# Kernel optimization log

Measured on AMD Instinct MI355X. Metric: run time of the kernel, lower is better.

Reference implementation:

```python
import jax, jax.numpy as jnp
import numpy as np

B, S, D, H = 2, 2048, 1024, 16
DK = D // H

def setup_inputs() -> dict:
    key = jax.random.key(0)
    ks = jax.random.split(key, 11)
    s = 1.0 / np.sqrt(D)
    return {
        "q": jax.random.normal(ks[0], (B, S, D), jnp.float32),
        "k": jax.random.normal(ks[1], (B, S, D), jnp.float32),
        "v": jax.random.normal(ks[2], (B, S, D), jnp.float32),
        "Wq": jax.random.normal(ks[3], (D, D), jnp.float32) * s,
        "bq": jax.random.normal(ks[4], (D,), jnp.float32) * s,
        "Wk": jax.random.normal(ks[5], (D, D), jnp.float32) * s,
        "bk": jax.random.normal(ks[6], (D,), jnp.float32) * s,
        "Wv": jax.random.normal(ks[7], (D, D), jnp.float32) * s,
        "bv": jax.random.normal(ks[8], (D,), jnp.float32) * s,
        "Wo": jax.random.normal(ks[9], (D, D), jnp.float32) * s,
        "bo": jax.random.normal(ks[10], (D,), jnp.float32) * s,
    }

def reference(q, k, v, Wq, bq, Wk, bk, Wv, bv, Wo, bo):
    # Linear projections, then split into heads: [B,S,D] -> [B,H,S,DK]
    def heads(x, W, b):
        y = x @ W.T + b
        return y.reshape(B, S, H, DK).transpose(0, 2, 1, 3)
    qh = heads(q, Wq, bq)
    kh = heads(k, Wk, bk)
    vh = heads(v, Wv, bv)
    scores = jnp.einsum('bhsd,bhtd->bhst', qh, kh) / jnp.sqrt(jnp.float32(DK))
    attn = jax.nn.softmax(scores, axis=-1)
    out = jnp.einsum('bhst,bhtd->bhsd', attn, vh)  # [B,H,S,DK]
    out = out.transpose(0, 2, 1, 3).reshape(B, S, D)
    return out @ Wo.T + bo
```

## Files before the change

kernel.cpp:

```cpp
#include <hip/hip_runtime.h>
#include <stdint.h>

#define B_  2
#define S_  2048
#define D_  1024
#define H_  16
#define DK_ 64

typedef unsigned short u16;
typedef __attribute__((ext_vector_type(8))) __bf16 bf16x8;
typedef __attribute__((ext_vector_type(4))) float f32x4;
typedef __attribute__((ext_vector_type(16))) float f32x16;
typedef __attribute__((ext_vector_type(4))) short short4v;
typedef __attribute__((ext_vector_type(8))) short short8v;

static __device__ __forceinline__ u16 f2bf(float f) {
    union { float f; uint32_t u; } v; v.f = f;
    return (u16)((v.u + 0x7fffu + ((v.u >> 16) & 1u)) >> 16);
}
static __device__ __forceinline__ uint32_t pk2bf(float x, float y) {
    return (uint32_t)f2bf(x) | ((uint32_t)f2bf(y) << 16);
}
static __device__ __forceinline__ uint32_t cvtpk_bf16(float lo, float hi) {
    uint32_t r; asm("v_cvt_pk_bf16_f32 %0, %1, %2" : "=v"(r) : "v"(lo), "v"(hi));
    return r;
}
static __device__ __forceinline__ float exp2f_fast(float x) {
    float r; asm("v_exp_f32 %0, %1" : "=v"(r) : "v"(x)); return r;
}

#define GLOAD16(gp, lp) \
    __builtin_amdgcn_global_load_lds((const __attribute__((address_space(1))) void*)(gp), \
                                     (__attribute__((address_space(3))) void*)(lp), 16, 0, 0)

static __device__ __forceinline__ int swz(int lin) { return lin ^ ((lin >> 3) & 7); }
static __device__ __forceinline__ int swz2(int lin) {
    return lin ^ ((lin >> 3) & 7) ^ ((lin >> 6) & 3);
}

static __device__ __forceinline__ int xcd_swz(int bid, int cpx) {
    return (bid & 7) * cpx + (bid >> 3);
}

__global__ __launch_bounds__(256) void cast_all_kernel(
        const float* __restrict__ q, const float* __restrict__ k, const float* __restrict__ v,
        const float* __restrict__ Wq, const float* __restrict__ Wk,
        const float* __restrict__ Wv, const float* __restrict__ Wo,
        u16* __restrict__ qb, u16* __restrict__ kb, u16* __restrict__ vb,
        u16* __restrict__ Wqb, u16* __restrict__ Wkb, u16* __restrict__ Wvb,
        u16* __restrict__ Wob) {
    int blk = blockIdx.x;
    const float* src; u16* dst; int off;
    if (blk < 2048)      { src = q;  dst = qb;  off = blk; }
    else if (blk < 4096) { src = k;  dst = kb;  off = blk - 2048; }
    else if (blk < 6144) { src = v;  dst = vb;  off = blk - 4096; }
    else if (blk < 6656) { src = Wq; dst = Wqb; off = blk - 6144; }
    else if (blk < 7168) { src = Wk; dst = Wkb; off = blk - 6656; }
    else if (blk < 7680) { src = Wv; dst = Wvb; off = blk - 7168; }
    else                 { src = Wo; dst = Wob; off = blk - 7680; }
    int i = (off * 256 + threadIdx.x) * 8;
    float4 a = *(const float4*)(src + i);
    float4 b = *(const float4*)(src + i + 4);
    uint4 r;
    r.x = pk2bf(a.x, a.y); r.y = pk2bf(a.z, a.w);
    r.z = pk2bf(b.x, b.y); r.w = pk2bf(b.z, b.w);
    *(uint4*)(void*)(dst + i) = r;
}

__device__ __forceinline__ void gemm128_compute(
        const u16* __restrict__ X, const u16* __restrict__ W,
        int m0, int n0, u16* lds, f32x4 acc[4][4]) {
    const int tid = threadIdx.x, lane = tid & 63, w = tid >> 6;
    const int wm = w >> 1, wn = w & 1;
    u16* As = lds;
    u16* Bs = lds + 8192;

    auto stage = [&](int bi, int kt) {
#pragma unroll
        for (int r = 0; r < 2; ++r) {
            int s = tid + (r << 8);
            int lin = s ^ ((s >> 3) & 7);
            int row = lin >> 2, ch = lin & 3;
            GLOAD16(X + (size_t)(m0 + row) * 1024 + (kt << 5) + (ch << 3),
                    (char*)(As + bi * 4096) + ((r << 8) + (w << 6)) * 16);
            GLOAD16(W + (size_t)(n0 + row) * 1024 + (kt << 5) + (ch << 3),
                    (char*)(Bs + bi * 4096) + ((r << 8) + (w << 6)) * 16);
        }
    };

    stage(0, 0);
    asm volatile("s_waitcnt vmcnt(0)" ::: "memory");
    __syncthreads();
#pragma unroll 1
    for (int kt = 0; kt < 32; ++kt) {
        const int cur = kt & 1;
        if (kt < 31) stage(cur ^ 1, kt + 1);
        const char* Ab = (const char*)(As + cur * 4096);
        const char* Bb = (const char*)(Bs + cur * 4096);
        bf16x8 a[4], b[4];
#pragma unroll
        for (int f = 0; f < 4; ++f) {
            int rowa = wm * 64 + f * 16 + (lane & 15);
            a[f] = *(const bf16x8*)(Ab + swz(rowa * 4 + (lane >> 4)) * 16);
            int rowb = wn * 64 + f * 16 + (lane & 15);
            b[f] = *(const bf16x8*)(Bb + swz(rowb * 4 + (lane >> 4)) * 16);
        }
#pragma unroll
        for (int fm = 0; fm < 4; ++fm)
#pragma unroll
            for (int fn = 0; fn < 4; ++fn)
                acc[fm][fn] = __builtin_amdgcn_mfma_f32_16x16x32_bf16(
                    a[fm], b[fn], acc[fm][fn], 0, 0, 0);
        __syncthreads();
    }
}

__device__ __forceinline__ void stage_half(const u16* __restrict__ src,
        int R0, int kt, u16* dst, int tid) {
#pragma unroll
    for (int r = 0; r < 2; ++r) {
        int s = tid + (r << 9);
        int lin = s ^ ((s >> 3) & 7);
        int row = lin >> 3, ch = lin & 7;
        GLOAD16(src + (size_t)(R0 + row) * 1024 + (kt << 6) + (ch << 3),
                (char*)dst + ((r << 9) + ((tid >> 6) << 6)) * 16);
    }
}

#define VM4  asm volatile("s_waitcnt vmcnt(4)" ::: "memory")
#define VM0  asm volatile("s_waitcnt vmcnt(0)" ::: "memory")

#define PHASE(QQ, MP, LOADB, STAGE_STMT, VM_STMT)                                \
    {                                                                            \
        bf16x8 afr[2][2];                                                        \
        if (LOADB) {                                                             \
            _Pragma("unroll") for (int fn = 0; fn < 4; ++fn)                     \
            _Pragma("unroll") for (int ks = 0; ks < 2; ++ks) {                   \
                int lin = (brow0 + fn * 16 + (lane & 15)) * 8 + ks * 4 + (lane >> 4); \
                bfr[fn][ks] = *(const bf16x8*)(Bhb[QQ] + swz(lin) * 16);         \
            }                                                                    \
        }                                                                        \
        _Pragma("unroll") for (int fo = 0; fo < 2; ++fo)                         \
        _Pragma("unroll") for (int ks = 0; ks < 2; ++ks) {                       \
            int lin = ((MP) * 32 + fo * 16 + (lane & 15)) * 8 + ks * 4 + (lane >> 4); \
            afr[fo][ks] = *(const bf16x8*)(Ahb[QQ] + swz(lin) * 16);             \
        }                                                                        \
        STAGE_STMT;                                                              \
        VM_STMT;                                                                 \
        __builtin_amdgcn_s_barrier();                                            \
        __builtin_amdgcn_sched_barrier(0);                                       \
        __builtin_amdgcn_s_setprio(1);                                           \
        _Pragma("unroll") for (int fo = 0; fo < 2; ++fo)                         \
        _Pragma("unroll") for (int ks = 0; ks < 2; ++ks)                         \
        _Pragma("unroll") for (int fn = 0; fn < 4; ++fn)                         \
            acc[(MP) * 2 + fo][fn] = __builtin_amdgcn_mfma_f32_16x16x32_bf16(    \
                afr[fo][ks], bfr[fn][ks], acc[(MP) * 2 + fo][fn], 0, 0, 0);      \
        __builtin_amdgcn_s_setprio(0);                                           \
        __builtin_amdgcn_s_barrier();                                            \
        __builtin_amdgcn_sched_barrier(0);                                       \
    }

__global__ __launch_bounds__(512, 2) void qkv256_kernel(
        const u16* __restrict__ qX, const u16* __restrict__ kX, const u16* __restrict__ vX,
        const u16* __restrict__ Wq, const u16* __restrict__ Wk, const u16* __restrict__ Wv,
        const float* __restrict__ bq, const float* __restrict__ bk, const float* __restrict__ bv,
        u16* __restrict__ qo, u16* __restrict__ ko, u16* __restrict__ vt) {
    __shared__ __align__(16) u16 lds[65536];
    const int tid = threadIdx.x, lane = tid & 63, w = tid >> 6;
    const int wm = w >> 2, wn = w & 3;
    const int lg = xcd_swz(blockIdx.x, 24);
    const int which = lg >> 6;
    const int rem = lg & 63;
    const int n0 = (rem >> 4) << 8;
    const int m0 = (rem & 15) << 8;
    const u16* X = which == 0 ? qX : (which == 1 ? kX : vX);
    const u16* W = which == 0 ? Wq : (which == 1 ? Wk : Wv);
    const float* bias = which == 0 ? bq : (which == 1 ? bk : bv);

    u16* Abase = lds;
    u16* Bbase = lds + 32768;

    stage_half(X, m0,        0, Abase + 0,             tid);
    stage_half(X, m0 + 128,  0, Abase + 8192,          tid);
    stage_half(W, n0,        0, Bbase + 0,             tid);
    stage_half(W, n0 + 128,  0, Bbase + 8192,          tid);
    stage_half(W, n0,        1, Bbase + 16384,         tid);
    stage_half(W, n0 + 128,  1, Bbase + 16384 + 8192,  tid);
    VM4;
    __builtin_amdgcn_s_barrier();
    __builtin_amdgcn_sched_barrier(0);

    f32x4 acc[8][4] = {};
    bf16x8 bfr[4][2];
    const char* Ahb[2] = { (const char*)(Abase + wm * 8192),
                           (const char*)(Abase + 16384 + wm * 8192) };
    const char* Bhb[2] = { (const char*)(Bbase + (wn >> 1) * 8192),
                           (const char*)(Bbase + 16384 + (wn >> 1) * 8192) };
    const int brow0 = (wn & 1) * 64;

#pragma unroll 1
    for (int i = 0; i < 8; ++i) {
        const int t0 = 2 * i, t1 = 2 * i + 1;
        const bool nl = (i < 7);
        PHASE(0, 0, true,  stage_half(X, m0,       t1,     Abase + 16384,        tid), (void)0);
        PHASE(0, 1, false, stage_half(X, m0 + 128, t1,     Abase + 16384 + 8192, tid), (void)0);
        PHASE(0, 2, false, if (nl) stage_half(W, n0,       t0 + 2, Bbase + 0,    tid), (void)0);
        PHASE(0, 3, false, if (nl) stage_half(W, n0 + 128, t0 + 2, Bbase + 8192, tid),
              if (nl) { VM4; } else { VM0; });
        PHASE(1, 0, true,  if (nl) stage_half(X, m0,       t0 + 2, Abase + 0,    tid), (void)0);
        PHASE(1, 1, false, if (nl) stage_half(X, m0 + 128, t0 + 2, Abase + 8192, tid), (void)0);
        PHASE(1, 2, false, if (nl) stage_half(W, n0,       t1 + 2, Bbase + 16384, tid), (void)0);
        PHASE(1, 3, false, if (nl) stage_half(W, n0 + 128, t1 + 2, Bbase + 16384 + 8192, tid),
              if (nl) { VM4; });
    }

    if (which < 2) {
        u16* out = which == 0 ? qo : ko;
        const float scale = which == 0 ? 0.1803368801111883f : 1.0f;
#pragma unroll
        for (int fn = 0; fn < 4; ++fn) {
            int n = n0 + wn * 64 + fn * 16 + (lane & 15);
            float bb = bias[n];
            int h = n >> 6, dk = n & 63;
#pragma unroll
            for (int fm = 0; fm < 8; ++fm)
#pragma unroll
                for (int j = 0; j < 4; ++j) {
                    int m = m0 + wm * 128 + fm * 16 + (lane >> 4) * 4 + j;
                    int b = m >> 11, s = m & 2047;
                    out[((size_t)(b * H_ + h) * S_ + s) * DK_ + dk] =
                        f2bf((acc[fm][fn][j] + bb) * scale);
                }
        }
    } else {
        __syncthreads();
        u16* wl = lds + w * 8192;
#pragma unroll
        for (int fn = 0; fn < 4; ++fn) {
            int dk = fn * 16 + (lane & 15);
            float bb = bias[n0 + wn * 64 + dk];
            int xr = (dk & 7) << 3;
#pragma unroll
            for (int fm = 0; fm < 8; ++fm) {
                int sl = fm * 16 + (lane >> 4) * 4;
                short4v p;
#pragma unroll
                for (int j = 0; j < 4; ++j) p[j] = (short)f2bf(acc[fm][fn][j] + bb);
                *(short4v*)(void*)&wl[dk * 128 + (sl ^ xr)] = p;
            }
        }
        int mrow = m0 + wm * 128;
        int b = mrow >> 11, sbase = mrow & 2047;
        int h = (n0 >> 6) + wn;
        u16* dst = vt + ((size_t)(b * H_ + h) * DK_) * S_ + sbase;
#pragma unroll
        for (int oc = 0; oc < 8; ++oc)
#pragma unroll
            for (int ic = 0; ic < 2; ++ic) {
                int dk = oc * 8 + (lane >> 3);
                int sc = ic * 8 + (lane & 7);
                short8v vv = *(const short8v*)(const void*)
                    &wl[dk * 128 + ((sc * 8) ^ ((dk & 7) << 3))];
                *(short8v*)(void*)(dst + (size_t)dk * S_ + sc * 8) = vv;
            }
    }
}

__global__ __launch_bounds__(256) void oproj_kernel(
        const u16* __restrict__ X, const u16* __restrict__ W,
        const float* __restrict__ bias, float* __restrict__ out) {
    __shared__ __align__(16) u16 lds[16384];
    const int bid = xcd_swz(blockIdx.x, 32);
    const int m0 = (bid >> 3) << 7;
    const int n0 = (bid & 7) << 7;
    f32x4 acc[4][4] = {};
    gemm128_compute(X, W, m0, n0, lds, acc);

    const int lane = threadIdx.x & 63, w = threadIdx.x >> 6;
    const int wm = w >> 1, wn = w & 1;
#pragma unroll
    for (int fn = 0; fn < 4; ++fn) {
        int n = n0 + wn * 64 + fn * 16 + (lane & 15);
        float bb = bias[n];
#pragma unroll
        for (int fm = 0; fm < 4; ++fm)
#pragma unroll
            for (int j = 0; j < 4; ++j) {
                int m = m0 + wm * 64 + fm * 16 + (lane >> 4) * 4 + j;
                out[(size_t)m * 1024 + n] = acc[fm][fn][j] + bb;
            }
    }
}

__global__ __launch_bounds__(256, 2) void attn_kernel(
        const u16* __restrict__ qh, const u16* __restrict__ kh,
        const u16* __restrict__ Vt, u16* __restrict__ ao) {
    __shared__ __align__(16) u16 Qs[8192];
    __shared__ __align__(16) u16 Ks[4][4096];
    __shared__ __align__(16) u16 Vs[4][4096];

    const int tid = threadIdx.x, lane = tid & 63, w = tid >> 6;
    const int l31 = lane & 31, hh = lane >> 5;
    const int lg = xcd_swz(blockIdx.x, 64);
    const int bh = lg >> 4, qt = lg & 15;
    const u16* qg = qh + ((size_t)bh * S_ + qt * 128) * DK_;
    const u16* kg = kh + (size_t)bh * S_ * DK_;
    const u16* vg = Vt + (size_t)bh * DK_ * S_;

    auto stageKV = [&](int slot, int kt) {
#pragma unroll
        for (int r = 0; r < 2; ++r) {
            int s = tid + (r << 8);
            int lin = swz2(s);
            int row = lin >> 3, ch = lin & 7;
            GLOAD16(kg + (size_t)(kt * 64 + row) * 64 + (ch << 3),
                    (char*)(&Ks[slot][0]) + ((r << 8) + (w << 6)) * 16);
            GLOAD16(vg + (size_t)row * S_ + kt * 64 + (ch << 3),
                    (char*)(&Vs[slot][0]) + ((r << 8) + (w << 6)) * 16);
        }
    };

#pragma unroll
    for (int r = 0; r < 4; ++r) {
        int s = tid + (r << 8);
        int lin = swz2(s);
        int row = lin >> 3, ch = lin & 7;
        GLOAD16(qg + row * 64 + (ch << 3), (char*)Qs + ((r << 8) + (w << 6)) * 16);
    }
    stageKV(0, 0);
    stageKV(1, 1);
    asm volatile("s_waitcnt vmcnt(0)" ::: "memory");
    __syncthreads();

    bf16x8 qf[4];
#pragma unroll
    for (int c = 0; c < 4; ++c) {
        int row = w * 32 + l31;
        qf[c] = *(const bf16x8*)((const char*)Qs + swz2(row * 8 + c * 2 + hh) * 16);
    }

    f32x16 acc[2] = {};
    float rs = 0.f;

#define ATTN_TILE(SLOT, PAOUT)                                                   \
    {                                                                            \
        const char* Kb = (const char*)&Ks[SLOT][0];                              \
        f32x16 st[2] = {};                                                       \
        _Pragma("unroll") for (int kb = 0; kb < 2; ++kb) {                       \
            bf16x8 kf[4];                                                        \
            _Pragma("unroll") for (int c = 0; c < 4; ++c) {                      \
                int row = kb * 32 + l31;                                         \
                kf[c] = *(const bf16x8*)(Kb + swz2(row * 8 + c * 2 + hh) * 16);  \
            }                                                                    \
            __builtin_amdgcn_s_setprio(1);                                       \
            _Pragma("unroll") for (int c = 0; c < 4; ++c)                        \
                st[kb] = __builtin_amdgcn_mfma_f32_32x32x16_bf16(                \
                    kf[c], qf[c], st[kb], 0, 0, 0);                              \
            __builtin_amdgcn_s_setprio(0);                                       \
        }                                                                        \
        _Pragma("unroll") for (int c = 0; c < 4; ++c) {                          \
            const int kb = c >> 1, o = (c & 1) * 8;                              \
            float e0 = exp2f_fast(st[kb][o + 0]);                                \
            float e1 = exp2f_fast(st[kb][o + 1]);                                \
            float e2 = exp2f_fast(st[kb][o + 2]);                                \
            float e3 = exp2f_fast(st[kb][o + 3]);                                \
            float e4 = exp2f_fast(st[kb][o + 4]);                                \
            float e5 = exp2f_fast(st[kb][o + 5]);                                \
            float e6 = exp2f_fast(st[kb][o + 6]);                                \
            float e7 = exp2f_fast(st[kb][o + 7]);                                \
            rs += ((e0 + e1) + (e2 + e3)) + ((e4 + e5) + (e6 + e7));             \
            uint32_t u0 = cvtpk_bf16(e0, e1);                                    \
            uint32_t u1 = cvtpk_bf16(e2, e3);                                    \
            uint32_t u2 = cvtpk_bf16(e4, e5);                                    \
            uint32_t u3 = cvtpk_bf16(e6, e7);                                    \
            asm volatile("v_permlane32_swap_b32 %0, %1" : "+v"(u0), "+v"(u2));   \
            asm volatile("v_permlane32_swap_b32 %0, %1" : "+v"(u1), "+v"(u3));   \
            union { uint32_t u[4]; bf16x8 v; } pu;                               \
            pu.u[0] = u0; pu.u[1] = u1; pu.u[2] = u2; pu.u[3] = u3;              \
            PAOUT[c] = pu.v;                                                     \
        }                                                                        \
        const char* Vb = (const char*)&Vs[SLOT][0];                              \
        _Pragma("unroll") for (int nb = 0; nb < 2; ++nb) {                       \
            bf16x8 vf[4];                                                        \
            _Pragma("unroll") for (int c = 0; c < 4; ++c) {                      \
                int row = nb * 32 + l31;                                         \
                vf[c] = *(const bf16x8*)(Vb + swz2(row * 8 + c * 2 + hh) * 16);  \
            }                                                                    \
            __builtin_amdgcn_s_setprio(1);                                       \
            _Pragma("unroll") for (int c = 0; c < 4; ++c)                        \
                acc[nb] = __builtin_amdgcn_mfma_f32_32x32x16_bf16(               \
                    PAOUT[c], vf[c], acc[nb], 0, 0, 0);                          \
            __builtin_amdgcn_s_setprio(0);                                       \
        }                                                                        \
    }

#pragma unroll 1
    for (int i = 0; i < 16; ++i) {
        const int t = 2 * i;
        if (i < 15) {
            stageKV((t + 2) & 3, t + 2);
            stageKV((t + 3) & 3, t + 3);
        }
        bf16x8 pa0[4], pa1[4];
        ATTN_TILE((t) & 3, pa0);
        ATTN_TILE((t + 1) & 3, pa1);
        __syncthreads();
    }
#undef ATTN_TILE

    rs += __shfl_xor(rs, 32);
    const int bb = bh >> 4, hd = bh & 15;
#pragma unroll
    for (int r = 0; r < 16; ++r) {
        int ql = (r & 3) + 8 * (r >> 2) + 4 * hh;
        float inv = 1.0f / __shfl(rs, ql);
        int srow = qt * 128 + w * 32 + ql;
#pragma unroll
        for (int nb = 0; nb < 2; ++nb) {
            int col = hd * 64 + nb * 32 + l31;
            ao[((size_t)bb * S_ + srow) * D_ + col] = f2bf(acc[nb][r] * inv);
        }
    }
}

extern "C" void kernel_launch(void* const* d_in, const int* in_sizes, int n_in,
                              void* d_out, int out_size, void* d_ws, size_t ws_size,
                              hipStream_t stream) {
    const float* q  = (const float*)d_in[0];
    const float* k  = (const float*)d_in[1];
    const float* v  = (const float*)d_in[2];
    const float* Wq = (const float*)d_in[3];
    const float* bq = (const float*)d_in[4];
    const float* Wk = (const float*)d_in[5];
    const float* bk = (const float*)d_in[6];
    const float* Wv = (const float*)d_in[7];
    const float* bv = (const float*)d_in[8];
    const float* Wo = (const float*)d_in[9];
    const float* bo = (const float*)d_in[10];

    char* ws = (char*)d_ws;
    u16* qb  = (u16*)(ws);
    u16* kb  = (u16*)(ws + (8u  << 20));
    u16* vb  = (u16*)(ws + (16u << 20));
    u16* Wqb = (u16*)(ws + (24u << 20));
    u16* Wkb = (u16*)(ws + (26u << 20));
    u16* Wvb = (u16*)(ws + (28u << 20));
    u16* Wob = (u16*)(ws + (30u << 20));
    u16* qhb = (u16*)(ws + (32u << 20));
    u16* khb = (u16*)(ws + (40u << 20));
    u16* Vtb = (u16*)(ws + (48u << 20));
    u16* aob = kb;

    cast_all_kernel<<<8192, 256, 0, stream>>>(q, k, v, Wq, Wk, Wv, Wo,
                                              qb, kb, vb, Wqb, Wkb, Wvb, Wob);

    qkv256_kernel<<<192, 512, 0, stream>>>(
        qb, kb, vb, Wqb, Wkb, Wvb, bq, bk, bv, qhb, khb, Vtb);

    attn_kernel<<<512, 256, 0, stream>>>(qhb, khb, Vtb, aob);

    oproj_kernel<<<256, 256, 0, stream>>>(aob, Wob, bo, (float*)d_out);
}
```

Before: 115.4 us.

## Split attention over two KV halves with a combine kernel

Adds a split-KV attention kernel in which each block handles half of the key sequence for one 128-query tile. This doubles the grid to 1024 blocks to improve occupancy across CUs. Each block writes unnormalized fp32 partial outputs and row sums, and a separate combine kernel adds the two halves, normalizes and casts to bf16. The cost is extra global traffic for the fp32 partials (about 32MB written then read) plus one more launch. The softmax has no max subtraction, so the halves can simply be summed. The new path runs only when the workspace is at least 91MB, otherwise it falls back to the original kernel.

```diff
diff --git a/kernel.cpp b/kernel.cpp
--- a/kernel.cpp
+++ b/kernel.cpp
@@ -423,6 +423,149 @@
     }
 }
 
+__global__ __launch_bounds__(256, 4) void attn_split_kernel(
+        const u16* __restrict__ qh, const u16* __restrict__ kh,
+        const u16* __restrict__ Vt, float* __restrict__ Opart,
+        float* __restrict__ rspart) {
+    __shared__ __align__(16) u16 Ks[2][4096];
+    __shared__ __align__(16) u16 Vs[2][4096];
+
+    const int tid = threadIdx.x, lane = tid & 63, w = tid >> 6;
+    const int l31 = lane & 31, hh = lane >> 5;
+    const int lg = xcd_swz(blockIdx.x, 128);
+    const int bh = lg >> 5;
+    const int kvh = (lg >> 4) & 1;
+    const int qt = lg & 15;
+    const int kb0 = kvh * 16;
+    const u16* qg = qh + ((size_t)bh * S_ + qt * 128) * DK_;
+    const u16* kg = kh + (size_t)bh * S_ * DK_;
+    const u16* vg = Vt + (size_t)bh * DK_ * S_;
+
+    auto stageKV = [&](int slot, int kt) {
+#pragma unroll
+        for (int r = 0; r < 2; ++r) {
+            int s = tid + (r << 8);
+            int lin = swz2(s);
+            int row = lin >> 3, ch = lin & 7;
+            GLOAD16(kg + (size_t)(kt * 64 + row) * 64 + (ch << 3),
+                    (char*)(&Ks[slot][0]) + ((r << 8) + (w << 6)) * 16);
+            GLOAD16(vg + (size_t)row * S_ + kt * 64 + (ch << 3),
+                    (char*)(&Vs[slot][0]) + ((r << 8) + (w << 6)) * 16);
+        }
+    };
+
+    stageKV(0, kb0);
+    bf16x8 qf[4];
+#pragma unroll
+    for (int c = 0; c < 4; ++c)
+        qf[c] = *(const bf16x8*)(qg + (size_t)(w * 32 + l31) * 64 + c * 16 + hh * 8);
+    asm volatile("s_waitcnt vmcnt(0)" ::: "memory");
+    __syncthreads();
+
+    f32x16 acc[2] = {};
+    float rs = 0.f;
+
+#pragma unroll 1
+    for (int i = 0; i < 16; ++i) {
+        const int cur = i & 1;
+        if (i < 15) stageKV(cur ^ 1, kb0 + i + 1);
+        const char* Kb = (const char*)&Ks[cur][0];
+        f32x16 st[2] = {};
+#pragma unroll
+        for (int kb = 0; kb < 2; ++kb) {
+            bf16x8 kf[4];
+#pragma unroll
+            for (int c = 0; c < 4; ++c) {
+                int row = kb * 32 + l31;
+                kf[c] = *(const bf16x8*)(Kb + swz2(row * 8 + c * 2 + hh) * 16);
+            }
+            __builtin_amdgcn_s_setprio(1);
+#pragma unroll
+            for (int c = 0; c < 4; ++c)
+                st[kb] = __builtin_amdgcn_mfma_f32_32x32x16_bf16(
+                    kf[c], qf[c], st[kb], 0, 0, 0);
+            __builtin_amdgcn_s_setprio(0);
+        }
+        bf16x8 pa[4];
+#pragma unroll
+        for (int c = 0; c < 4; ++c) {
+            const int kb = c >> 1, o = (c & 1) * 8;
+            float e0 = exp2f_fast(st[kb][o + 0]);
+            float e1 = exp2f_fast(st[kb][o + 1]);
+            float e2 = exp2f_fast(st[kb][o + 2]);
+            float e3 = exp2f_fast(st[kb][o + 3]);
+            float e4 = exp2f_fast(st[kb][o + 4]);
+            float e5 = exp2f_fast(st[kb][o + 5]);
+            float e6 = exp2f_fast(st[kb][o + 6]);
+            float e7 = exp2f_fast(st[kb][o + 7]);
+            rs += ((e0 + e1) + (e2 + e3)) + ((e4 + e5) + (e6 + e7));
+            uint32_t u0 = cvtpk_bf16(e0, e1);
+            uint32_t u1 = cvtpk_bf16(e2, e3);
+            uint32_t u2 = cvtpk_bf16(e4, e5);
+            uint32_t u3 = cvtpk_bf16(e6, e7);
+            asm volatile("v_permlane32_swap_b32 %0, %1" : "+v"(u0), "+v"(u2));
+            asm volatile("v_permlane32_swap_b32 %0, %1" : "+v"(u1), "+v"(u3));
+            union { uint32_t u[4]; bf16x8 v; } pu;
+            pu.u[0] = u0; pu.u[1] = u1; pu.u[2] = u2; pu.u[3] = u3;
+            pa[c] = pu.v;
+        }
+        const char* Vb = (const char*)&Vs[cur][0];
+#pragma unroll
+        for (int nb = 0; nb < 2; ++nb) {
+            bf16x8 vf[4];
+#pragma unroll
+            for (int c = 0; c < 4; ++c) {
+                int row = nb * 32 + l31;
+                vf[c] = *(const bf16x8*)(Vb + swz2(row * 8 + c * 2 + hh) * 16);
+            }
+            __builtin_amdgcn_s_setprio(1);
+#pragma unroll
+            for (int c = 0; c < 4; ++c)
+                acc[nb] = __builtin_amdgcn_mfma_f32_32x32x16_bf16(
+                    pa[c], vf[c], acc[nb], 0, 0, 0);
+            __builtin_amdgcn_s_setprio(0);
+        }
+        __syncthreads();
+    }
+
+    rs += __shfl_xor(rs, 32);
+    const int bb = bh >> 4, hd = bh & 15;
+    if (hh == 0)
+        rspart[((size_t)kvh * 32 + bh) * S_ + qt * 128 + w * 32 + l31] = rs;
+    float* Ob = Opart + (size_t)kvh * B_ * S_ * D_;
+#pragma unroll
+    for (int r = 0; r < 16; ++r) {
+        int ql = (r & 3) + 8 * (r >> 2) + 4 * hh;
+        int srow = qt * 128 + w * 32 + ql;
+#pragma unroll
+        for (int nb = 0; nb < 2; ++nb) {
+            int col = hd * 64 + nb * 32 + l31;
+            Ob[((size_t)bb * S_ + srow) * D_ + col] = acc[nb][r];
+        }
+    }
+}
+
+__global__ __launch_bounds__(256) void combine_kernel(
+        const float* __restrict__ Opart, const float* __restrict__ rspart,
+        u16* __restrict__ ao) {
+    const int bs = blockIdx.x;
+    const int b = bs >> 11, s = bs & 2047;
+    const int d = threadIdx.x * 4;
+    const int bh = b * 16 + (d >> 6);
+    float r0 = rspart[(size_t)bh * S_ + s];
+    float r1 = rspart[(size_t)(32 + bh) * S_ + s];
+    float inv = 1.0f / (r0 + r1);
+    size_t off = ((size_t)b * S_ + s) * D_ + d;
+    float4 o0 = *(const float4*)(Opart + off);
+    float4 o1 = *(const float4*)(Opart + (size_t)B_ * S_ * D_ + off);
+    short4v r;
+    r[0] = (short)f2bf((o0.x + o1.x) * inv);
+    r[1] = (short)f2bf((o0.y + o1.y) * inv);
+    r[2] = (short)f2bf((o0.z + o1.z) * inv);
+    r[3] = (short)f2bf((o0.w + o1.w) * inv);
+    *(short4v*)(void*)(ao + off) = r;
+}
+
 extern "C" void kernel_launch(void* const* d_in, const int* in_sizes, int n_in,
                               void* d_out, int out_size, void* d_ws, size_t ws_size,
                               hipStream_t stream) {
@@ -450,6 +593,8 @@
     u16* khb = (u16*)(ws + (40u << 20));
     u16* Vtb = (u16*)(ws + (48u << 20));
     u16* aob = kb;
+    float* Opart  = (float*)(ws + (56u << 20));
+    float* rspart = (float*)(ws + (90u << 20));
 
     cast_all_kernel<<<8192, 256, 0, stream>>>(q, k, v, Wq, Wk, Wv, Wo,
                                               qb, kb, vb, Wqb, Wkb, Wvb, Wob);
@@ -457,7 +602,12 @@
     qkv256_kernel<<<192, 512, 0, stream>>>(
         qb, kb, vb, Wqb, Wkb, Wvb, bq, bk, bv, qhb, khb, Vtb);
 
-    attn_kernel<<<512, 256, 0, stream>>>(qhb, khb, Vtb, aob);
+    if (ws_size >= (91ull << 20)) {
+        attn_split_kernel<<<1024, 256, 0, stream>>>(qhb, khb, Vtb, Opart, rspart);
+        combine_kernel<<<4096, 256, 0, stream>>>(Opart, rspart, aob);
+    } else {
+        attn_kernel<<<512, 256, 0, stream>>>(qhb, khb, Vtb, aob);
+    }
 
     oproj_kernel<<<256, 256, 0, stream>>>(aob, Wob, bo, (float*)d_out);
 }
```

Result: slower. 121.9 us (+5.6%).
